# Performance work log

Hardware: AMD Instinct MI355X
Metric: run time of the kernel (lower is better)

The kernel has to match this reference:

```python
import jax, jax.numpy as jnp
import numpy as np

N_NODES = 100000
N_EDGES = 1600000
IN_DIM = 128
HEADS = 2
OUT_DIM = 64


def setup_inputs() -> dict:
    key = jax.random.key(0)
    k1, k2, k3, k4, k5 = jax.random.split(key, 5)
    x = jax.random.normal(k1, (N_NODES, IN_DIM), dtype=jnp.float32)
    edge_index = jax.random.randint(k2, (2, N_EDGES), 0, N_NODES, dtype=jnp.int32)
    # xavier-uniform-ish scales
    W = jax.random.uniform(k3, (IN_DIM, HEADS * OUT_DIM), dtype=jnp.float32,
                           minval=-1.0, maxval=1.0) * (6.0 / (IN_DIM + HEADS * OUT_DIM)) ** 0.5
    attn_l = jax.random.uniform(k4, (HEADS, OUT_DIM), dtype=jnp.float32,
                                minval=-1.0, maxval=1.0) * (6.0 / (HEADS + OUT_DIM)) ** 0.5
    attn_r = jax.random.uniform(k5, (HEADS, OUT_DIM), dtype=jnp.float32,
                                minval=-1.0, maxval=1.0) * (6.0 / (HEADS + OUT_DIM)) ** 0.5
    return {"x": x, "edge_index": edge_index, "W": W, "attn_l": attn_l, "attn_r": attn_r}


def reference(x, edge_index, W, attn_l, attn_r):
    N = x.shape[0]
    h = (x @ W).reshape(N, HEADS, OUT_DIM)          # [N,H,D]
    src, dst = edge_index[0], edge_index[1]          # [E]
    h_src = h[src]                                   # [E,H,D] gather
    h_dst = h[dst]                                   # [E,H,D] gather
    # per-edge, per-head attention logits
    alpha = jnp.einsum('ehd,hd->eh', h_src, attn_l) + jnp.einsum('ehd,hd->eh', h_dst, attn_r)
    alpha = jax.nn.leaky_relu(alpha, negative_slope=0.2)
    # NOTE: faithful to original torch code: softmax over dim=0 (ALL edges per head)
    alpha = jax.nn.softmax(alpha, axis=0)            # [E,H]
    msg = h_src * alpha[:, :, None]                  # [E,H,D]
    out = jnp.zeros((N, HEADS, OUT_DIM), dtype=h.dtype).at[dst].add(msg)
    return out.reshape(N, HEADS * OUT_DIM)
```

## Files before the change

kernel.cpp:

```cpp
#include <hip/hip_runtime.h>
#include <hip/hip_fp16.h>
#include <math.h>

#define IN_DIM   128
#define HEADS    2
#define OUT_DIM  64
#define OCOLS    128
#define NB_A     1024
#define BSHIFT   8
#define MAXB     512
#define PCOPIES  8
#define CAP      6144
#define PARTB    128
#define LOG2E    1.4426950408889634f

typedef __attribute__((ext_vector_type(4))) _Float16 half4v;
typedef __attribute__((ext_vector_type(8))) _Float16 half8v;
typedef __attribute__((ext_vector_type(4))) float    floatx4;

__global__ __launch_bounds__(256) void pack_w_kernel(
    const float* __restrict__ W, half8v* __restrict__ wpack) {
  int t = threadIdx.x;
  for (int s = t; s < 2048; s += 256) {
    int l = s & 63, ct = (s >> 6) & 7, kk = s >> 9;
    int q = l >> 4, n = l & 15;
    int c = ct * 16 + n;
    half8v f;
#pragma unroll
    for (int j = 0; j < 8; j++) {
      f[j] = (_Float16)W[(size_t)(kk * 32 + q * 8 + j) * OCOLS + c];
    }
    wpack[s] = f;
  }
}

__global__ __launch_bounds__(256) void gemm_kernel(
    const float* __restrict__ x, const half8v* __restrict__ wpack,
    const float* __restrict__ attn_l, const float* __restrict__ attn_r,
    _Float16* __restrict__ h16, float* __restrict__ alr, int N) {
  __shared__ half8v Wlds[2048];
  __shared__ __align__(16) _Float16 hstage[64 * OCOLS];
  const int tid = threadIdx.x;
  for (int i = tid; i < 2048; i += 256) Wlds[i] = wpack[i];

  const int wave = tid >> 6, lane = tid & 63;
  const int q = lane >> 4, m = lane & 15;
  const int rbase = blockIdx.x * 64 + wave * 16;
  const int arow = rbase + m;
  const bool rok = arow < N;

  half8v a[4];
#pragma unroll
  for (int kk = 0; kk < 4; kk++) {
    float4 u = rok ? *(const float4*)&x[(size_t)arow * IN_DIM + kk * 32 + q * 8]
                   : make_float4(0.f, 0.f, 0.f, 0.f);
    float4 v = rok ? *(const float4*)&x[(size_t)arow * IN_DIM + kk * 32 + q * 8 + 4]
                   : make_float4(0.f, 0.f, 0.f, 0.f);
    a[kk][0] = (_Float16)u.x; a[kk][1] = (_Float16)u.y;
    a[kk][2] = (_Float16)u.z; a[kk][3] = (_Float16)u.w;
    a[kk][4] = (_Float16)v.x; a[kk][5] = (_Float16)v.y;
    a[kk][6] = (_Float16)v.z; a[kk][7] = (_Float16)v.w;
  }
  __syncthreads();

  floatx4 acc[8];
#pragma unroll
  for (int ct = 0; ct < 8; ct++) {
    floatx4 c = {0.f, 0.f, 0.f, 0.f};
#pragma unroll
    for (int kk = 0; kk < 4; kk++) {
      c = __builtin_amdgcn_mfma_f32_16x16x32_f16(
          a[kk], Wlds[(kk * 8 + ct) * 64 + lane], c, 0, 0, 0);
    }
    acc[ct] = c;
  }

  float Al[8], Ar[8];
#pragma unroll
  for (int ct = 0; ct < 8; ct++) {
    Al[ct] = attn_l[ct * 16 + m];
    Ar[ct] = attn_r[ct * 16 + m];
  }
#pragma unroll
  for (int r = 0; r < 4; r++) {
    float al0 = 0.f, al1 = 0.f, ar0 = 0.f, ar1 = 0.f;
#pragma unroll
    for (int ct = 0; ct < 4; ct++) {
      al0 += acc[ct][r] * Al[ct];
      ar0 += acc[ct][r] * Ar[ct];
      al1 += acc[ct + 4][r] * Al[ct + 4];
      ar1 += acc[ct + 4][r] * Ar[ct + 4];
    }
#pragma unroll
    for (int off = 1; off < 16; off <<= 1) {
      al0 += __shfl_xor(al0, off);
      al1 += __shfl_xor(al1, off);
      ar0 += __shfl_xor(ar0, off);
      ar1 += __shfl_xor(ar1, off);
    }
    int orow = rbase + q * 4 + r;
    if (m == 0 && orow < N) {
      *(float4*)&alr[(size_t)orow * 4] =
          make_float4(al0 * LOG2E, al1 * LOG2E, ar0 * LOG2E, ar1 * LOG2E);
    }
  }

#pragma unroll
  for (int ct = 0; ct < 8; ct++) {
#pragma unroll
    for (int r = 0; r < 4; r++) {
      hstage[(wave * 16 + q * 4 + r) * OCOLS + ct * 16 + m] = (_Float16)acc[ct][r];
    }
  }
  __syncthreads();
  {
    int srow = tid >> 2, seg = tid & 3;
    int grow = blockIdx.x * 64 + srow;
    if (grow < N) {
      const int4* s = (const int4*)&hstage[srow * OCOLS + seg * 32];
      int4* d = (int4*)&h16[(size_t)grow * OCOLS + seg * 32];
      int4 v0 = s[0], v1 = s[1], v2 = s[2], v3 = s[3];
      d[0] = v0; d[1] = v1; d[2] = v2; d[3] = v3;
    }
  }
}

__device__ inline void softmax_comb(float& m, float& s, float m2, float s2) {
  float M = fmaxf(m, m2);
  s = s * __builtin_amdgcn_exp2f(m - M) + s2 * __builtin_amdgcn_exp2f(m2 - M);
  m = M;
}

__global__ __launch_bounds__(256) void alpha_stats_kernel(
    const int* __restrict__ src, const int* __restrict__ dst,
    const float* __restrict__ alr, float* __restrict__ partials,
    int* __restrict__ bucket_cnt, int E, int nb1) {
  __shared__ int hist[MAXB];
  for (int i = threadIdx.x; i < MAXB; i += 256) hist[i] = 0;
  __syncthreads();
  const char* ab = (const char*)alr;
  float m0 = -1e30f, s0 = 0.f, m1 = -1e30f, s1 = 0.f;
  for (int e = blockIdx.x * 256 + threadIdx.x; e < E; e += gridDim.x * 256) {
    int sn = src[e], dn = dst[e];
    atomicAdd(&hist[dn >> BSHIFT], 1);
    float4 as = *(const float4*)(ab + ((unsigned)sn << 4));
    float4 ad = *(const float4*)(ab + ((unsigned)dn << 4));
    float a0 = as.x + ad.z;
    float a1 = as.y + ad.w;
    a0 = (a0 > 0.f) ? a0 : 0.2f * a0;
    a1 = (a1 > 0.f) ? a1 : 0.2f * a1;
    {
      float M = fmaxf(m0, a0);
      s0 = s0 * __builtin_amdgcn_exp2f(m0 - M) + __builtin_amdgcn_exp2f(a0 - M);
      m0 = M;
    }
    {
      float M = fmaxf(m1, a1);
      s1 = s1 * __builtin_amdgcn_exp2f(m1 - M) + __builtin_amdgcn_exp2f(a1 - M);
      m1 = M;
    }
  }
  __syncthreads();
  for (int b = threadIdx.x; b < nb1; b += 256) {
    int h = hist[b];
    if (h) atomicAdd(&bucket_cnt[(blockIdx.x & (PCOPIES - 1)) * MAXB + b], h);
  }
#pragma unroll
  for (int off = 1; off < 64; off <<= 1) {
    float m0o = __shfl_xor(m0, off), s0o = __shfl_xor(s0, off);
    float m1o = __shfl_xor(m1, off), s1o = __shfl_xor(s1, off);
    softmax_comb(m0, s0, m0o, s0o);
    softmax_comb(m1, s1, m1o, s1o);
  }
  __shared__ float red[4][4];
  int wave = threadIdx.x >> 6;
  int lane = threadIdx.x & 63;
  if (lane == 0) {
    red[wave][0] = m0; red[wave][1] = s0; red[wave][2] = m1; red[wave][3] = s1;
  }
  __syncthreads();
  if (threadIdx.x == 0) {
    float M0 = red[0][0], S0 = red[0][1], M1 = red[0][2], S1 = red[0][3];
    for (int w = 1; w < 4; w++) {
      softmax_comb(M0, S0, red[w][0], red[w][1]);
      softmax_comb(M1, S1, red[w][2], red[w][3]);
    }
    float* p = &partials[(size_t)blockIdx.x * 4];
    p[0] = M0; p[1] = S0; p[2] = M1; p[3] = S1;
  }
}

__global__ __launch_bounds__(256) void reduce_kernel(
    const float* __restrict__ partials, float* __restrict__ stats) {
  float m0 = -1e30f, s0 = 0.f, m1 = -1e30f, s1 = 0.f;
  for (int i = threadIdx.x; i < NB_A; i += 256) {
    const float* p = &partials[(size_t)i * 4];
    softmax_comb(m0, s0, p[0], p[1]);
    softmax_comb(m1, s1, p[2], p[3]);
  }
#pragma unroll
  for (int off = 1; off < 64; off <<= 1) {
    float m0o = __shfl_xor(m0, off), s0o = __shfl_xor(s0, off);
    float m1o = __shfl_xor(m1, off), s1o = __shfl_xor(s1, off);
    softmax_comb(m0, s0, m0o, s0o);
    softmax_comb(m1, s1, m1o, s1o);
  }
  __shared__ float red[4][4];
  int wave = threadIdx.x >> 6;
  int lane = threadIdx.x & 63;
  if (lane == 0) {
    red[wave][0] = m0; red[wave][1] = s0; red[wave][2] = m1; red[wave][3] = s1;
  }
  __syncthreads();
  if (threadIdx.x == 0) {
    float M0 = red[0][0], S0 = red[0][1], M1 = red[0][2], S1 = red[0][3];
    for (int w = 1; w < 4; w++) {
      softmax_comb(M0, S0, red[w][0], red[w][1]);
      softmax_comb(M1, S1, red[w][2], red[w][3]);
    }
    stats[0] = M0; stats[1] = 1.f / S0;
    stats[2] = M1; stats[3] = 1.f / S1;
  }
}

__global__ __launch_bounds__(512) void bucket_scan_kernel(
    const int* __restrict__ bucket_cnt, int* __restrict__ bucket_off,
    int* __restrict__ bucket_cursor, int nb1) {
  __shared__ int part[512];
  int t = threadIdx.x;
  int v = 0;
  if (t < nb1) {
#pragma unroll
    for (int c = 0; c < PCOPIES; c++) v += bucket_cnt[c * MAXB + t];
  }
  part[t] = v;
  __syncthreads();
  for (int d = 1; d < 512; d <<= 1) {
    int x = (t >= d) ? part[t - d] : 0;
    __syncthreads();
    part[t] += x;
    __syncthreads();
  }
  int excl = part[t] - v;
  if (t < nb1) {
    bucket_off[t] = excl;
    bucket_cursor[t] = excl;
  }
  if (t == 511) bucket_off[nb1] = part[511];
}

__global__ __launch_bounds__(256) void partition_kernel(
    const int* __restrict__ src, const int* __restrict__ dst,
    int* __restrict__ bucket_cursor, unsigned int* __restrict__ pairs,
    int E, int nb1, int chunk) {
  __shared__ int hist[MAXB];
  __shared__ int cur[MAXB];
  int base = blockIdx.x * chunk;
  int lim = min(base + chunk, E);
  for (int i = threadIdx.x; i < MAXB; i += 256) hist[i] = 0;
  __syncthreads();
  for (int e = base + threadIdx.x; e < lim; e += 256) {
    atomicAdd(&hist[dst[e] >> BSHIFT], 1);
  }
  __syncthreads();
  for (int b = threadIdx.x; b < nb1; b += 256) {
    cur[b] = atomicAdd(&bucket_cursor[b], hist[b]);
  }
  __syncthreads();
  for (int e = base + threadIdx.x; e < lim; e += 256) {
    int d = dst[e];
    int slot = atomicAdd(&cur[d >> BSHIFT], 1);
    pairs[slot] = (unsigned int)src[e] | ((unsigned int)(d & 255) << 17);
  }
}

__global__ __launch_bounds__(256) void bucket_csr_kernel(
    const unsigned int* __restrict__ pairs, const int* __restrict__ bucket_off,
    int* __restrict__ off, int* __restrict__ edge_src, int N, int nb1) {
  __shared__ int hist[256];
  __shared__ int cur[256];
  __shared__ int buf[CAP];
  int b = blockIdx.x;
  int t = threadIdx.x;
  int base_node = b << BSHIFT;
  int nn = min(256, N - base_node);
  int pbeg = bucket_off[b], pend = bucket_off[b + 1];
  int cntE = pend - pbeg;

  hist[t] = 0;
  __syncthreads();
  for (int i = t; i < cntE; i += 256) {
    atomicAdd(&hist[pairs[pbeg + i] >> 17], 1);
  }
  __syncthreads();
  int v = hist[t];
  for (int d = 1; d < 256; d <<= 1) {
    int x = (t >= d) ? hist[t - d] : 0;
    __syncthreads();
    hist[t] += x;
    __syncthreads();
  }
  int excl = hist[t] - v;
  cur[t] = excl;
  if (t < nn) off[base_node + t] = pbeg + excl;
  if (b == nb1 - 1 && t == 0) off[N] = pend;
  __syncthreads();
  if (cntE <= CAP) {
    for (int i = t; i < cntE; i += 256) {
      unsigned int p = pairs[pbeg + i];
      int slot = atomicAdd(&cur[p >> 17], 1);
      buf[slot] = (int)(p & 0x1FFFFu);
    }
    __syncthreads();
    for (int i = t; i < cntE; i += 256) {
      edge_src[pbeg + i] = buf[i];
    }
  } else {
    for (int i = t; i < cntE; i += 256) {
      unsigned int p = pairs[pbeg + i];
      int slot = atomicAdd(&cur[p >> 17], 1);
      edge_src[pbeg + slot] = (int)(p & 0x1FFFFu);
    }
  }
}

__global__ __launch_bounds__(256) void gather_kernel(
    const int* __restrict__ off, const int* __restrict__ edge_src,
    const float* __restrict__ alr, const float* __restrict__ stats,
    const _Float16* __restrict__ h16, float* __restrict__ out, int N) {
  int gid = blockIdx.x * 256 + threadIdx.x;
  int n = gid >> 6;
  if (n >= N) return;
  int lane = threadIdx.x & 63;
  int sub = lane >> 4;
  int l = lane & 15;
  int head = l >> 3;

  const char* ab = (const char*)alr;
  const char* hb = (const char*)h16;
  float4 ad = *(const float4*)(ab + ((unsigned)n << 4));
  float adv = head ? ad.w : ad.z;
  float M = stats[head * 2];
  float invS = stats[head * 2 + 1];
  unsigned loff = (unsigned)l * 16u;

  int beg = off[n], end = off[n + 1];
  float acc[8] = {0.f, 0.f, 0.f, 0.f, 0.f, 0.f, 0.f, 0.f};
  int i = beg + sub;
  for (; i + 4 < end; i += 8) {
    int sn0 = edge_src[i], sn1 = edge_src[i + 4];
    float4 as0 = *(const float4*)(ab + ((unsigned)sn0 << 4));
    float4 as1 = *(const float4*)(ab + ((unsigned)sn1 << 4));
    half8v hv0 = *(const half8v*)(hb + (((unsigned)sn0 << 8) + loff));
    half8v hv1 = *(const half8v*)(hb + (((unsigned)sn1 << 8) + loff));
    float a0 = (head ? as0.y : as0.x) + adv;
    float a1 = (head ? as1.y : as1.x) + adv;
    a0 = (a0 > 0.f) ? a0 : 0.2f * a0;
    a1 = (a1 > 0.f) ? a1 : 0.2f * a1;
    float w0 = __builtin_amdgcn_exp2f(a0 - M) * invS;
    float w1 = __builtin_amdgcn_exp2f(a1 - M) * invS;
#pragma unroll
    for (int j = 0; j < 8; j++) acc[j] += w0 * (float)hv0[j];
#pragma unroll
    for (int j = 0; j < 8; j++) acc[j] += w1 * (float)hv1[j];
  }
  if (i < end) {
    int sn = edge_src[i];
    float4 as = *(const float4*)(ab + ((unsigned)sn << 4));
    half8v hv = *(const half8v*)(hb + (((unsigned)sn << 8) + loff));
    float a = (head ? as.y : as.x) + adv;
    a = (a > 0.f) ? a : 0.2f * a;
    float w = __builtin_amdgcn_exp2f(a - M) * invS;
#pragma unroll
    for (int j = 0; j < 8; j++) acc[j] += w * (float)hv[j];
  }
#pragma unroll
  for (int j = 0; j < 8; j++) {
    acc[j] += __shfl_xor(acc[j], 16);
    acc[j] += __shfl_xor(acc[j], 32);
  }
  if (sub == 0) {
    char* ob = (char*)out;
    unsigned obase = ((unsigned)n << 9) + (unsigned)l * 32u;
    *(float4*)(ob + obase)      = make_float4(acc[0], acc[1], acc[2], acc[3]);
    *(float4*)(ob + obase + 16) = make_float4(acc[4], acc[5], acc[6], acc[7]);
  }
}

extern "C" void kernel_launch(void* const* d_in, const int* in_sizes, int n_in,
                              void* d_out, int out_size, void* d_ws, size_t ws_size,
                              hipStream_t stream) {
  const float* x      = (const float*)d_in[0];
  const int*   edge   = (const int*)d_in[1];
  const float* W      = (const float*)d_in[2];
  const float* attn_l = (const float*)d_in[3];
  const float* attn_r = (const float*)d_in[4];

  const int N = in_sizes[0] / IN_DIM;
  const int E = in_sizes[1] / 2;
  const int* src = edge;
  const int* dst = edge + E;
  float* out = (float*)d_out;

  const int nb1 = (N + 255) >> BSHIFT;

  _Float16*     h16      = (_Float16*)d_ws;
  float*        alr      = (float*)(h16 + (size_t)N * OCOLS);
  float*        partials = alr + (size_t)N * 4;
  float*        stats    = partials + (size_t)NB_A * 4;
  int*          bucket_cnt    = (int*)(stats + 4);
  int*          bucket_off    = bucket_cnt + PCOPIES * MAXB;
  int*          bucket_cursor = bucket_off + MAXB + 1;
  int*          off      = bucket_cursor + MAXB;
  unsigned int* pairs    = (unsigned int*)(off + N + 1);
  int*          edge_src = (int*)(pairs + E);
  half8v*       wpack    = (half8v*)(edge_src + E);

  const int chunk = (E + PARTB - 1) / PARTB;

  hipMemsetAsync(bucket_cnt, 0, PCOPIES * MAXB * sizeof(int), stream);

  pack_w_kernel<<<1, 256, 0, stream>>>(W, wpack);
  gemm_kernel<<<(N + 63) / 64, 256, 0, stream>>>(x, wpack, attn_l, attn_r, h16, alr, N);
  alpha_stats_kernel<<<NB_A, 256, 0, stream>>>(src, dst, alr, partials, bucket_cnt, E, nb1);
  reduce_kernel<<<1, 256, 0, stream>>>(partials, stats);
  bucket_scan_kernel<<<1, 512, 0, stream>>>(bucket_cnt, bucket_off, bucket_cursor, nb1);
  partition_kernel<<<PARTB, 256, 0, stream>>>(src, dst, bucket_cursor, pairs, E, nb1, chunk);
  bucket_csr_kernel<<<nb1, 256, 0, stream>>>(pairs, bucket_off, off, edge_src, N, nb1);
  gather_kernel<<<((size_t)N * 64 + 255) / 256, 256, 0, stream>>>(
      off, edge_src, alr, stats, h16, out, N);
}
```

Measured before the change: 283.5 us.

## Fuse CSR build with gather, use upper-bound softmax max, drop reduce kernel

The gemm kernel now computes per-column maxima of the attention logits and atomically maxes them, so the softmax stats pass becomes a plain exp-sum against a fixed upper-bound max. The separate reduce kernel is merged into the bucket scan. The partition kernel reuses per-block histograms instead of recounting. Buckets shrink to 128 nodes, and a new kernel fuses the per-bucket CSR sort with the gather, precomputing fp16 edge weights with a 2^14 scale. This removes two launches and the edge_src round trip through global memory. The cost is added fp16 weight quantisation and overflow/underflow risk from the scaled bound.

```diff
diff --git a/kernel.cpp b/kernel.cpp
--- a/kernel.cpp
+++ b/kernel.cpp
@@ -4,23 +4,38 @@
 
 #define IN_DIM   128
 #define HEADS    2
-#define OUT_DIM  64
 #define OCOLS    128
 #define NB_A     1024
-#define BSHIFT   8
-#define MAXB     512
+#define BSHIFT   7
+#define BNODES   128
+#define MAXB     1024
 #define PCOPIES  8
-#define CAP      6144
+#define CAP      2560
 #define PARTB    128
+#define SCALE    14.0f
 #define LOG2E    1.4426950408889634f
 
-typedef __attribute__((ext_vector_type(4))) _Float16 half4v;
 typedef __attribute__((ext_vector_type(8))) _Float16 half8v;
+typedef __attribute__((ext_vector_type(2))) _Float16 half2v;
 typedef __attribute__((ext_vector_type(4))) float    floatx4;
 
+union h2u { half2v h; int i; };
+
+__device__ inline unsigned fkey(float f) {
+  unsigned u = __float_as_uint(f);
+  return (u & 0x80000000u) ? ~u : (u | 0x80000000u);
+}
+__device__ inline float fdecode(unsigned k) {
+  unsigned u = (k & 0x80000000u) ? (k & 0x7FFFFFFFu) : ~k;
+  return __uint_as_float(u);
+}
+
 __global__ __launch_bounds__(256) void pack_w_kernel(
-    const float* __restrict__ W, half8v* __restrict__ wpack) {
+    const float* __restrict__ W, half8v* __restrict__ wpack,
+    int* __restrict__ bucket_cnt, unsigned* __restrict__ maxkeys) {
   int t = threadIdx.x;
+  for (int i = t; i < PCOPIES * MAXB; i += 256) bucket_cnt[i] = 0;
+  if (t < 4) maxkeys[t] = 0u;
   for (int s = t; s < 2048; s += 256) {
     int l = s & 63, ct = (s >> 6) & 7, kk = s >> 9;
     int q = l >> 4, n = l & 15;
@@ -37,9 +52,11 @@
 __global__ __launch_bounds__(256) void gemm_kernel(
     const float* __restrict__ x, const half8v* __restrict__ wpack,
     const float* __restrict__ attn_l, const float* __restrict__ attn_r,
-    _Float16* __restrict__ h16, float* __restrict__ alr, int N) {
+    _Float16* __restrict__ h16, float* __restrict__ alr,
+    unsigned* __restrict__ maxkeys, int N) {
   __shared__ half8v Wlds[2048];
   __shared__ __align__(16) _Float16 hstage[64 * OCOLS];
+  __shared__ float bm[4][4];
   const int tid = threadIdx.x;
   for (int i = tid; i < 2048; i += 256) Wlds[i] = wpack[i];
 
@@ -81,6 +98,7 @@
     Al[ct] = attn_l[ct * 16 + m];
     Ar[ct] = attn_r[ct * 16 + m];
   }
+  float wm0 = -1e30f, wm1 = -1e30f, wm2 = -1e30f, wm3 = -1e30f;
 #pragma unroll
   for (int r = 0; r < 4; r++) {
     float al0 = 0.f, al1 = 0.f, ar0 = 0.f, ar1 = 0.f;
@@ -98,12 +116,19 @@
       ar0 += __shfl_xor(ar0, off);
       ar1 += __shfl_xor(ar1, off);
     }
+    wm0 = fmaxf(wm0, al0); wm1 = fmaxf(wm1, al1);
+    wm2 = fmaxf(wm2, ar0); wm3 = fmaxf(wm3, ar1);
     int orow = rbase + q * 4 + r;
     if (m == 0 && orow < N) {
       *(float4*)&alr[(size_t)orow * 4] =
           make_float4(al0 * LOG2E, al1 * LOG2E, ar0 * LOG2E, ar1 * LOG2E);
     }
   }
+  wm0 = fmaxf(wm0, __shfl_xor(wm0, 16)); wm0 = fmaxf(wm0, __shfl_xor(wm0, 32));
+  wm1 = fmaxf(wm1, __shfl_xor(wm1, 16)); wm1 = fmaxf(wm1, __shfl_xor(wm1, 32));
+  wm2 = fmaxf(wm2, __shfl_xor(wm2, 16)); wm2 = fmaxf(wm2, __shfl_xor(wm2, 32));
+  wm3 = fmaxf(wm3, __shfl_xor(wm3, 16)); wm3 = fmaxf(wm3, __shfl_xor(wm3, 32));
+  if (lane == 0) { bm[wave][0] = wm0; bm[wave][1] = wm1; bm[wave][2] = wm2; bm[wave][3] = wm3; }
 
 #pragma unroll
   for (int ct = 0; ct < 8; ct++) {
@@ -113,6 +138,13 @@
     }
   }
   __syncthreads();
+  if (tid == 0) {
+#pragma unroll
+    for (int c = 0; c < 4; c++) {
+      float mx = fmaxf(fmaxf(bm[0][c], bm[1][c]), fmaxf(bm[2][c], bm[3][c]));
+      atomicMax(&maxkeys[c], fkey(mx * LOG2E));
+    }
+  }
   {
     int srow = tid >> 2, seg = tid & 3;
     int grow = blockIdx.x * 64 + srow;
@@ -125,108 +157,54 @@
   }
 }
 
-__device__ inline void softmax_comb(float& m, float& s, float m2, float s2) {
-  float M = fmaxf(m, m2);
-  s = s * __builtin_amdgcn_exp2f(m - M) + s2 * __builtin_amdgcn_exp2f(m2 - M);
-  m = M;
-}
-
 __global__ __launch_bounds__(256) void alpha_stats_kernel(
     const int* __restrict__ src, const int* __restrict__ dst,
-    const float* __restrict__ alr, float* __restrict__ partials,
-    int* __restrict__ bucket_cnt, int E, int nb1) {
+    const float* __restrict__ alr, const unsigned* __restrict__ maxkeys,
+    float2* __restrict__ partials, int* __restrict__ bucket_cnt,
+    int* __restrict__ blockhist, int E, int nb1) {
   __shared__ int hist[MAXB];
   for (int i = threadIdx.x; i < MAXB; i += 256) hist[i] = 0;
   __syncthreads();
+  const float M0 = fmaxf(fdecode(maxkeys[0]) + fdecode(maxkeys[2]), 0.f);
+  const float M1 = fmaxf(fdecode(maxkeys[1]) + fdecode(maxkeys[3]), 0.f);
   const char* ab = (const char*)alr;
-  float m0 = -1e30f, s0 = 0.f, m1 = -1e30f, s1 = 0.f;
-  for (int e = blockIdx.x * 256 + threadIdx.x; e < E; e += gridDim.x * 256) {
+  float s0 = 0.f, s1 = 0.f;
+  for (int e = blockIdx.x * 256 + threadIdx.x; e < E; e += NB_A * 256) {
     int sn = src[e], dn = dst[e];
     atomicAdd(&hist[dn >> BSHIFT], 1);
-    float4 as = *(const float4*)(ab + ((unsigned)sn << 4));
-    float4 ad = *(const float4*)(ab + ((unsigned)dn << 4));
-    float a0 = as.x + ad.z;
-    float a1 = as.y + ad.w;
-    a0 = (a0 > 0.f) ? a0 : 0.2f * a0;
-    a1 = (a1 > 0.f) ? a1 : 0.2f * a1;
-    {
-      float M = fmaxf(m0, a0);
-      s0 = s0 * __builtin_amdgcn_exp2f(m0 - M) + __builtin_amdgcn_exp2f(a0 - M);
-      m0 = M;
-    }
-    {
-      float M = fmaxf(m1, a1);
-      s1 = s1 * __builtin_amdgcn_exp2f(m1 - M) + __builtin_amdgcn_exp2f(a1 - M);
-      m1 = M;
-    }
-  }
-  __syncthreads();
-  for (int b = threadIdx.x; b < nb1; b += 256) {
-    int h = hist[b];
-    if (h) atomicAdd(&bucket_cnt[(blockIdx.x & (PCOPIES - 1)) * MAXB + b], h);
+    float2 as = *(const float2*)(ab + ((unsigned)sn << 4));
+    float2 ad = *(const float2*)(ab + ((unsigned)dn << 4) + 8);
+    float a0 = as.x + ad.x; a0 = fmaxf(a0, 0.2f * a0);
+    float a1 = as.y + ad.y; a1 = fmaxf(a1, 0.2f * a1);
+    s0 += __builtin_amdgcn_exp2f(a0 - M0);
+    s1 += __builtin_amdgcn_exp2f(a1 - M1);
+  }
+  __syncthreads();
+  for (int j = threadIdx.x; j < nb1; j += 256) {
+    int h = hist[j];
+    blockhist[(size_t)blockIdx.x * nb1 + j] = h;
+    if (h) atomicAdd(&bucket_cnt[(blockIdx.x & (PCOPIES - 1)) * MAXB + j], h);
   }
 #pragma unroll
   for (int off = 1; off < 64; off <<= 1) {
-    float m0o = __shfl_xor(m0, off), s0o = __shfl_xor(s0, off);
-    float m1o = __shfl_xor(m1, off), s1o = __shfl_xor(s1, off);
-    softmax_comb(m0, s0, m0o, s0o);
-    softmax_comb(m1, s1, m1o, s1o);
-  }
-  __shared__ float red[4][4];
-  int wave = threadIdx.x >> 6;
-  int lane = threadIdx.x & 63;
-  if (lane == 0) {
-    red[wave][0] = m0; red[wave][1] = s0; red[wave][2] = m1; red[wave][3] = s1;
-  }
+    s0 += __shfl_xor(s0, off);
+    s1 += __shfl_xor(s1, off);
+  }
+  __shared__ float red[4][2];
+  int wv = threadIdx.x >> 6, ln = threadIdx.x & 63;
+  if (ln == 0) { red[wv][0] = s0; red[wv][1] = s1; }
   __syncthreads();
   if (threadIdx.x == 0) {
-    float M0 = red[0][0], S0 = red[0][1], M1 = red[0][2], S1 = red[0][3];
-    for (int w = 1; w < 4; w++) {
-      softmax_comb(M0, S0, red[w][0], red[w][1]);
-      softmax_comb(M1, S1, red[w][2], red[w][3]);
-    }
-    float* p = &partials[(size_t)blockIdx.x * 4];
-    p[0] = M0; p[1] = S0; p[2] = M1; p[3] = S1;
-  }
-}
-
-__global__ __launch_bounds__(256) void reduce_kernel(
-    const float* __restrict__ partials, float* __restrict__ stats) {
-  float m0 = -1e30f, s0 = 0.f, m1 = -1e30f, s1 = 0.f;
-  for (int i = threadIdx.x; i < NB_A; i += 256) {
-    const float* p = &partials[(size_t)i * 4];
-    softmax_comb(m0, s0, p[0], p[1]);
-    softmax_comb(m1, s1, p[2], p[3]);
-  }
-#pragma unroll
-  for (int off = 1; off < 64; off <<= 1) {
-    float m0o = __shfl_xor(m0, off), s0o = __shfl_xor(s0, off);
-    float m1o = __shfl_xor(m1, off), s1o = __shfl_xor(s1, off);
-    softmax_comb(m0, s0, m0o, s0o);
-    softmax_comb(m1, s1, m1o, s1o);
-  }
-  __shared__ float red[4][4];
-  int wave = threadIdx.x >> 6;
-  int lane = threadIdx.x & 63;
-  if (lane == 0) {
-    red[wave][0] = m0; red[wave][1] = s0; red[wave][2] = m1; red[wave][3] = s1;
-  }
-  __syncthreads();
-  if (threadIdx.x == 0) {
-    float M0 = red[0][0], S0 = red[0][1], M1 = red[0][2], S1 = red[0][3];
-    for (int w = 1; w < 4; w++) {
-      softmax_comb(M0, S0, red[w][0], red[w][1]);
-      softmax_comb(M1, S1, red[w][2], red[w][3]);
-    }
-    stats[0] = M0; stats[1] = 1.f / S0;
-    stats[2] = M1; stats[3] = 1.f / S1;
-  }
-}
-
-__global__ __launch_bounds__(512) void bucket_scan_kernel(
-    const int* __restrict__ bucket_cnt, int* __restrict__ bucket_off,
-    int* __restrict__ bucket_cursor, int nb1) {
-  __shared__ int part[512];
+    partials[blockIdx.x] = make_float2(red[0][0] + red[1][0] + red[2][0] + red[3][0],
+                                       red[0][1] + red[1][1] + red[2][1] + red[3][1]);
+  }
+}
+
+__global__ __launch_bounds__(1024) void bucket_scan_kernel(
+    const int* __restrict__ bucket_cnt, const float2* __restrict__ partials,
+    const unsigned* __restrict__ maxkeys, int* __restrict__ bucket_off,
+    int* __restrict__ bucket_cursor, float* __restrict__ stats, int nb1) {
+  __shared__ int part[1024];
   int t = threadIdx.x;
   int v = 0;
   if (t < nb1) {
@@ -235,155 +213,157 @@
   }
   part[t] = v;
   __syncthreads();
-  for (int d = 1; d < 512; d <<= 1) {
+  for (int d = 1; d < 1024; d <<= 1) {
     int x = (t >= d) ? part[t - d] : 0;
     __syncthreads();
     part[t] += x;
     __syncthreads();
   }
   int excl = part[t] - v;
-  if (t < nb1) {
-    bucket_off[t] = excl;
-    bucket_cursor[t] = excl;
-  }
-  if (t == 511) bucket_off[nb1] = part[511];
+  if (t < nb1) { bucket_off[t] = excl; bucket_cursor[t] = excl; }
+  if (t == 1023) bucket_off[nb1] = part[1023];
+  float2 p = partials[t];
+  float s0 = p.x, s1 = p.y;
+#pragma unroll
+  for (int off = 1; off < 64; off <<= 1) {
+    s0 += __shfl_xor(s0, off);
+    s1 += __shfl_xor(s1, off);
+  }
+  __shared__ float red[16][2];
+  int wv = t >> 6, ln = t & 63;
+  if (ln == 0) { red[wv][0] = s0; red[wv][1] = s1; }
+  __syncthreads();
+  if (t == 0) {
+    float S0 = 0.f, S1 = 0.f;
+    for (int w = 0; w < 16; w++) { S0 += red[w][0]; S1 += red[w][1]; }
+    float M0 = fmaxf(fdecode(maxkeys[0]) + fdecode(maxkeys[2]), 0.f);
+    float M1 = fmaxf(fdecode(maxkeys[1]) + fdecode(maxkeys[3]), 0.f);
+    stats[0] = M0 - SCALE; stats[1] = 1.f / S0;
+    stats[2] = M1 - SCALE; stats[3] = 1.f / S1;
+  }
 }
 
 __global__ __launch_bounds__(256) void partition_kernel(
     const int* __restrict__ src, const int* __restrict__ dst,
-    int* __restrict__ bucket_cursor, unsigned int* __restrict__ pairs,
-    int E, int nb1, int chunk) {
-  __shared__ int hist[MAXB];
+    const int* __restrict__ blockhist, int* __restrict__ bucket_cursor,
+    unsigned* __restrict__ pairs, int E, int nb1) {
   __shared__ int cur[MAXB];
-  int base = blockIdx.x * chunk;
-  int lim = min(base + chunk, E);
-  for (int i = threadIdx.x; i < MAXB; i += 256) hist[i] = 0;
-  __syncthreads();
-  for (int e = base + threadIdx.x; e < lim; e += 256) {
-    atomicAdd(&hist[dst[e] >> BSHIFT], 1);
-  }
-  __syncthreads();
-  for (int b = threadIdx.x; b < nb1; b += 256) {
-    cur[b] = atomicAdd(&bucket_cursor[b], hist[b]);
-  }
-  __syncthreads();
-  for (int e = base + threadIdx.x; e < lim; e += 256) {
-    int d = dst[e];
-    int slot = atomicAdd(&cur[d >> BSHIFT], 1);
-    pairs[slot] = (unsigned int)src[e] | ((unsigned int)(d & 255) << 17);
-  }
-}
-
-__global__ __launch_bounds__(256) void bucket_csr_kernel(
-    const unsigned int* __restrict__ pairs, const int* __restrict__ bucket_off,
-    int* __restrict__ off, int* __restrict__ edge_src, int N, int nb1) {
-  __shared__ int hist[256];
-  __shared__ int cur[256];
-  __shared__ int buf[CAP];
-  int b = blockIdx.x;
-  int t = threadIdx.x;
-  int base_node = b << BSHIFT;
-  int nn = min(256, N - base_node);
-  int pbeg = bucket_off[b], pend = bucket_off[b + 1];
-  int cntE = pend - pbeg;
-
-  hist[t] = 0;
-  __syncthreads();
-  for (int i = t; i < cntE; i += 256) {
-    atomicAdd(&hist[pairs[pbeg + i] >> 17], 1);
-  }
-  __syncthreads();
-  int v = hist[t];
-  for (int d = 1; d < 256; d <<= 1) {
-    int x = (t >= d) ? hist[t - d] : 0;
+  const int t = threadIdx.x, p = blockIdx.x;
+  for (int j = t; j < nb1; j += 256) {
+    int s = 0;
+#pragma unroll
+    for (int k = 0; k < 8; k++) s += blockhist[(size_t)(8 * p + k) * nb1 + j];
+    cur[j] = s ? atomicAdd(&bucket_cursor[j], s) : 0;
+  }
+  __syncthreads();
+  for (int k = 0; k < 8; k++) {
+    int b = 8 * p + k;
+    for (int e = b * 256 + t; e < E; e += NB_A * 256) {
+      int sn = src[e], dn = dst[e];
+      int slot = atomicAdd(&cur[dn >> BSHIFT], 1);
+      pairs[slot] = (unsigned)sn | ((unsigned)(dn & (BNODES - 1)) << 17);
+    }
+  }
+}
+
+__global__ __launch_bounds__(512) void sortgather_kernel(
+    const unsigned* __restrict__ pairs, const int* __restrict__ bucket_off,
+    const float* __restrict__ alr, const float* __restrict__ stats,
+    const _Float16* __restrict__ h16, int2* __restrict__ gfall,
+    float* __restrict__ out, int N, int nb1) {
+  __shared__ unsigned pbuf[CAP];
+  __shared__ int2 buf[CAP];
+  __shared__ float2 adsh[BNODES];
+  __shared__ int hist[BNODES], scanv[BNODES], nodeoff[BNODES + 1], cur[BNODES];
+  const int b = blockIdx.x, t = threadIdx.x;
+  const int base = b << BSHIFT;
+  const int pbeg = bucket_off[b], pend = bucket_off[b + 1];
+  const int cntE = pend - pbeg;
+  const bool fits = (cntE <= CAP);
+
+  if (t < BNODES) {
+    hist[t] = 0;
+    int node = base + t;
+    if (node < N) {
+      const float* ap = (const float*)((const char*)alr + ((unsigned)node << 4));
+      adsh[t] = make_float2(ap[2], ap[3]);
+    }
+  }
+  __syncthreads();
+  if (fits) {
+    for (int i = t; i < cntE; i += 512) {
+      unsigned pr = pairs[pbeg + i];
+      pbuf[i] = pr;
+      atomicAdd(&hist[pr >> 17], 1);
+    }
+  } else {
+    for (int i = t; i < cntE; i += 512) atomicAdd(&hist[pairs[pbeg + i] >> 17], 1);
+  }
+  __syncthreads();
+  if (t < BNODES) scanv[t] = hist[t];
+  __syncthreads();
+  for (int d = 1; d < BNODES; d <<= 1) {
+    int x = (t >= d && t < BNODES) ? scanv[t - d] : 0;
     __syncthreads();
-    hist[t] += x;
+    if (t < BNODES) scanv[t] += x;
     __syncthreads();
   }
-  int excl = hist[t] - v;
-  cur[t] = excl;
-  if (t < nn) off[base_node + t] = pbeg + excl;
-  if (b == nb1 - 1 && t == 0) off[N] = pend;
-  __syncthreads();
-  if (cntE <= CAP) {
-    for (int i = t; i < cntE; i += 256) {
-      unsigned int p = pairs[pbeg + i];
-      int slot = atomicAdd(&cur[p >> 17], 1);
-      buf[slot] = (int)(p & 0x1FFFFu);
-    }
-    __syncthreads();
-    for (int i = t; i < cntE; i += 256) {
-      edge_src[pbeg + i] = buf[i];
-    }
-  } else {
-    for (int i = t; i < cntE; i += 256) {
-      unsigned int p = pairs[pbeg + i];
-      int slot = atomicAdd(&cur[p >> 17], 1);
-      edge_src[pbeg + slot] = (int)(p & 0x1FFFFu);
-    }
-  }
-}
-
-__global__ __launch_bounds__(256) void gather_kernel(
-    const int* __restrict__ off, const int* __restrict__ edge_src,
-    const float* __restrict__ alr, const float* __restrict__ stats,
-    const _Float16* __restrict__ h16, float* __restrict__ out, int N) {
-  int gid = blockIdx.x * 256 + threadIdx.x;
-  int n = gid >> 6;
-  if (n >= N) return;
-  int lane = threadIdx.x & 63;
-  int sub = lane >> 4;
-  int l = lane & 15;
-  int head = l >> 3;
-
+  if (t < BNODES) {
+    int ex = scanv[t] - hist[t];
+    nodeoff[t] = ex;
+    cur[t] = ex;
+  }
+  if (t == 0) nodeoff[BNODES] = cntE;
+  __syncthreads();
+  const float Madj0 = stats[0], invS0 = stats[1];
+  const float Madj1 = stats[2], invS1 = stats[3];
   const char* ab = (const char*)alr;
+  for (int i = t; i < cntE; i += 512) {
+    unsigned pr = fits ? pbuf[i] : pairs[pbeg + i];
+    int sn = (int)(pr & 0x1FFFFu);
+    int d = (int)(pr >> 17);
+    float2 as = *(const float2*)(ab + ((unsigned)sn << 4));
+    float2 ad = adsh[d];
+    float a0 = as.x + ad.x; a0 = fmaxf(a0, 0.2f * a0);
+    float a1 = as.y + ad.y; a1 = fmaxf(a1, 0.2f * a1);
+    float w0 = __builtin_amdgcn_exp2f(a0 - Madj0) * invS0;
+    float w1 = __builtin_amdgcn_exp2f(a1 - Madj1) * invS1;
+    h2u pk;
+    pk.h = half2v{(_Float16)w0, (_Float16)w1};
+    int slot = atomicAdd(&cur[d], 1);
+    int2 ent = make_int2(sn, pk.i);
+    if (fits) buf[slot] = ent;
+    else gfall[pbeg + slot] = ent;
+  }
+  __syncthreads();
+  const int wv = t >> 6, ln = t & 63;
+  const int sub = ln >> 4, l = ln & 15, head = l >> 3;
   const char* hb = (const char*)h16;
-  float4 ad = *(const float4*)(ab + ((unsigned)n << 4));
-  float adv = head ? ad.w : ad.z;
-  float M = stats[head * 2];
-  float invS = stats[head * 2 + 1];
-  unsigned loff = (unsigned)l * 16u;
-
-  int beg = off[n], end = off[n + 1];
-  float acc[8] = {0.f, 0.f, 0.f, 0.f, 0.f, 0.f, 0.f, 0.f};
-  int i = beg + sub;
-  for (; i + 4 < end; i += 8) {
-    int sn0 = edge_src[i], sn1 = edge_src[i + 4];
-    float4 as0 = *(const float4*)(ab + ((unsigned)sn0 << 4));
-    float4 as1 = *(const float4*)(ab + ((unsigned)sn1 << 4));
-    half8v hv0 = *(const half8v*)(hb + (((unsigned)sn0 << 8) + loff));
-    half8v hv1 = *(const half8v*)(hb + (((unsigned)sn1 << 8) + loff));
-    float a0 = (head ? as0.y : as0.x) + adv;
-    float a1 = (head ? as1.y : as1.x) + adv;
-    a0 = (a0 > 0.f) ? a0 : 0.2f * a0;
-    a1 = (a1 > 0.f) ? a1 : 0.2f * a1;
-    float w0 = __builtin_amdgcn_exp2f(a0 - M) * invS;
-    float w1 = __builtin_amdgcn_exp2f(a1 - M) * invS;
-#pragma unroll
-    for (int j = 0; j < 8; j++) acc[j] += w0 * (float)hv0[j];
-#pragma unroll
-    for (int j = 0; j < 8; j++) acc[j] += w1 * (float)hv1[j];
-  }
-  if (i < end) {
-    int sn = edge_src[i];
-    float4 as = *(const float4*)(ab + ((unsigned)sn << 4));
-    half8v hv = *(const half8v*)(hb + (((unsigned)sn << 8) + loff));
-    float a = (head ? as.y : as.x) + adv;
-    a = (a > 0.f) ? a : 0.2f * a;
-    float w = __builtin_amdgcn_exp2f(a - M) * invS;
-#pragma unroll
-    for (int j = 0; j < 8; j++) acc[j] += w * (float)hv[j];
-  }
-#pragma unroll
-  for (int j = 0; j < 8; j++) {
-    acc[j] += __shfl_xor(acc[j], 16);
-    acc[j] += __shfl_xor(acc[j], 32);
-  }
-  if (sub == 0) {
-    char* ob = (char*)out;
-    unsigned obase = ((unsigned)n << 9) + (unsigned)l * 32u;
-    *(float4*)(ob + obase)      = make_float4(acc[0], acc[1], acc[2], acc[3]);
-    *(float4*)(ob + obase + 16) = make_float4(acc[4], acc[5], acc[6], acc[7]);
+  const unsigned loff = (unsigned)l * 16u;
+  for (int n = wv; n < BNODES; n += 8) {
+    int beg = nodeoff[n], end = nodeoff[n + 1];
+    float acc[8] = {0.f, 0.f, 0.f, 0.f, 0.f, 0.f, 0.f, 0.f};
+    for (int i = beg + sub; i < end; i += 4) {
+      int2 ent = fits ? buf[i] : gfall[pbeg + i];
+      h2u pk; pk.i = ent.y;
+      float w = (float)(head ? pk.h.y : pk.h.x);
+      half8v hv = *(const half8v*)(hb + (((unsigned)ent.x << 8) + loff));
+#pragma unroll
+      for (int j = 0; j < 8; j++) acc[j] += w * (float)hv[j];
+    }
+#pragma unroll
+    for (int j = 0; j < 8; j++) {
+      acc[j] += __shfl_xor(acc[j], 16);
+      acc[j] += __shfl_xor(acc[j], 32);
+    }
+    int node = base + n;
+    if (sub == 0 && node < N) {
+      const float ds = 0x1.0p-14f;
+      char* ob = (char*)out;
+      unsigned obase = ((unsigned)node << 9) + (unsigned)l * 32u;
+      *(float4*)(ob + obase)      = make_float4(acc[0] * ds, acc[1] * ds, acc[2] * ds, acc[3] * ds);
+      *(float4*)(ob + obase + 16) = make_float4(acc[4] * ds, acc[5] * ds, acc[6] * ds, acc[7] * ds);
+    }
   }
 }
 
@@ -402,31 +382,33 @@
   const int* dst = edge + E;
   float* out = (float*)d_out;
 
-  const int nb1 = (N + 255) >> BSHIFT;
-
-  _Float16*     h16      = (_Float16*)d_ws;
-  float*        alr      = (float*)(h16 + (size_t)N * OCOLS);
-  float*        partials = alr + (size_t)N * 4;
-  float*        stats    = partials + (size_t)NB_A * 4;
-  int*          bucket_cnt    = (int*)(stats + 4);
-  int*          bucket_off    = bucket_cnt + PCOPIES * MAXB;
-  int*          bucket_cursor = bucket_off + MAXB + 1;
-  int*          off      = bucket_cursor + MAXB;
-  unsigned int* pairs    = (unsigned int*)(off + N + 1);
-  int*          edge_src = (int*)(pairs + E);
-  half8v*       wpack    = (half8v*)(edge_src + E);
-
-  const int chunk = (E + PARTB - 1) / PARTB;
-
-  hipMemsetAsync(bucket_cnt, 0, PCOPIES * MAXB * sizeof(int), stream);
-
-  pack_w_kernel<<<1, 256, 0, stream>>>(W, wpack);
-  gemm_kernel<<<(N + 63) / 64, 256, 0, stream>>>(x, wpack, attn_l, attn_r, h16, alr, N);
-  alpha_stats_kernel<<<NB_A, 256, 0, stream>>>(src, dst, alr, partials, bucket_cnt, E, nb1);
-  reduce_kernel<<<1, 256, 0, stream>>>(partials, stats);
-  bucket_scan_kernel<<<1, 512, 0, stream>>>(bucket_cnt, bucket_off, bucket_cursor, nb1);
-  partition_kernel<<<PARTB, 256, 0, stream>>>(src, dst, bucket_cursor, pairs, E, nb1, chunk);
-  bucket_csr_kernel<<<nb1, 256, 0, stream>>>(pairs, bucket_off, off, edge_src, N, nb1);
-  gather_kernel<<<((size_t)N * 64 + 255) / 256, 256, 0, stream>>>(
-      off, edge_src, alr, stats, h16, out, N);
-}
+  const int nb1 = (N + BNODES - 1) >> BSHIFT;
+
+  char* w = (char*)d_ws;
+  size_t o = 0;
+  _Float16* h16 = (_Float16*)(w + o);      o += (size_t)N * OCOLS * 2;
+  float*    alr = (float*)(w + o);         o += (size_t)N * 16;
+  float2*   partials = (float2*)(w + o);   o += (size_t)NB_A * 8;
+  float*    stats = (float*)(w + o);       o += 16;
+  unsigned* maxkeys = (unsigned*)(w + o);  o += 16;
+  int*      bucket_cnt = (int*)(w + o);    o += (size_t)PCOPIES * MAXB * 4;
+  int*      bucket_off = (int*)(w + o);    o += (size_t)(MAXB + 4) * 4;
+  int*      bucket_cursor = (int*)(w + o); o += (size_t)MAXB * 4;
+  int*      blockhist = (int*)(w + o);     o += (size_t)NB_A * nb1 * 4;
+  o = (o + 15) & ~(size_t)15;
+  unsigned* pairs = (unsigned*)(w + o);    o += (size_t)E * 4;
+  int2*     gfall = (int2*)(w + o);        o += (size_t)E * 8;
+  half8v*   wpack = (half8v*)(w + o);
+
+  pack_w_kernel<<<1, 256, 0, stream>>>(W, wpack, bucket_cnt, maxkeys);
+  gemm_kernel<<<(N + 63) / 64, 256, 0, stream>>>(x, wpack, attn_l, attn_r,
+                                                 h16, alr, maxkeys, N);
+  alpha_stats_kernel<<<NB_A, 256, 0, stream>>>(src, dst, alr, maxkeys,
+                                               partials, bucket_cnt, blockhist, E, nb1);
+  bucket_scan_kernel<<<1, 1024, 0, stream>>>(bucket_cnt, partials, maxkeys,
+                                             bucket_off, bucket_cursor, stats, nb1);
+  partition_kernel<<<PARTB, 256, 0, stream>>>(src, dst, blockhist, bucket_cursor,
+                                              pairs, E, nb1);
+  sortgather_kernel<<<nb1, 512, 0, stream>>>(pairs, bucket_off, alr, stats,
+                                             h16, gfall, out, N, nb1);
+}
```

Measured after the change: 309.6 us. 9.2% more time.
